# Kernel tuning notes

Hardware: AMD Instinct MI355X
Metric: run time of the kernel (lower is better)

The kernel has to match this reference:

```python
import jax, jax.numpy as jnp
import numpy as np

B, D_IN, D_HID, D_OUT, E = 8192, 1024, 4096, 1024, 8


def setup_inputs() -> dict:
    key = jax.random.key(0)
    ks = jax.random.split(key, 6)
    s_in = 1.0 / np.sqrt(D_IN)
    s_gh = 1.0 / np.sqrt(D_HID // 2)
    s_eh = 1.0 / np.sqrt(D_HID)
    return {
        "x": jax.random.normal(ks[0], (B, D_IN), jnp.float32),
        "gW1": jax.random.normal(ks[1], (D_IN, D_HID // 2), jnp.float32) * s_in,
        "gb1": jnp.zeros((D_HID // 2,), jnp.float32),
        "gW2": jax.random.normal(ks[2], (D_HID // 2, E), jnp.float32) * s_gh,
        "gb2": jnp.zeros((E,), jnp.float32),
        "eW1": jax.random.normal(ks[3], (E, D_IN, D_HID), jnp.float32) * s_in,
        "eb1": jnp.zeros((E, D_HID), jnp.float32),
        "eW2": jax.random.normal(ks[4], (E, D_HID, D_OUT), jnp.float32) * s_eh,
        "eb2": jnp.zeros((E, D_OUT), jnp.float32),
    }


def reference(x, gW1, gb1, gW2, gb2, eW1, eb1, eW2, eb2):
    # Gating network: Linear -> ReLU -> (Dropout: eval identity) -> Linear -> Softmax(dim=1)
    gh = jax.nn.relu(x @ gW1 + gb1)                      # [B, H/2]
    gates = jax.nn.softmax(gh @ gW2 + gb2, axis=1)       # [B, E]

    # All experts run on the full batch (dense MoE): batched GEMMs over expert axis.
    h = jax.nn.relu(jnp.einsum('bi,eih->beh', x, eW1) + eb1)   # [B, E, H]
    eo = jnp.einsum('beh,eho->beo', h, eW2) + eb2              # [B, E, O]

    # Gated weighted sum over experts.
    combined = jnp.einsum('beo,be->bo', eo, gates)             # [B, O]
    return (combined, gates, gates)
```

## Files before the change

kernel.cpp:

```cpp
#include <hip/hip_runtime.h>
#include <hip/hip_bf16.h>
#include <stdint.h>

#define BB 8192
#define DIN 1024
#define DHID 4096
#define DOUT 1024
#define NEXP 8
#define GH_N 2048

typedef __attribute__((ext_vector_type(8))) __bf16 bf16x8;
typedef __attribute__((ext_vector_type(4))) float f32x4;

__device__ inline unsigned short f2bf(float f) {
  unsigned u = __builtin_bit_cast(unsigned, f);
  u = (u + 0x7FFFu + ((u >> 16) & 1u)) >> 16;
  return (unsigned short)u;
}
__device__ inline float b2f(unsigned short s) {
  return __builtin_bit_cast(float, (unsigned)s << 16);
}

__global__ void cvt_f32_bf16(const float* __restrict__ in,
                             unsigned short* __restrict__ out, int n4) {
  int i = blockIdx.x * blockDim.x + threadIdx.x;
  if (i >= n4) return;
  float4 v = ((const float4*)in)[i];
  ushort4 o;
  o.x = f2bf(v.x); o.y = f2bf(v.y); o.z = f2bf(v.z); o.w = f2bf(v.w);
  ((ushort4*)out)[i] = o;
}

__device__ inline void tr_tile64(const float* __restrict__ in,
                                 unsigned short* __restrict__ out, int R, int C,
                                 int bx, int by) {
  __shared__ float tile[64][65];
  const int c0 = bx * 64, r0 = by * 64;
  const int tx = threadIdx.x & 63, ty = threadIdx.x >> 6;
#pragma unroll
  for (int i = 0; i < 16; ++i) {
    int r = i * 4 + ty;
    tile[r][tx] = in[(size_t)(r0 + r) * C + c0 + tx];
  }
  __syncthreads();
#pragma unroll
  for (int i = 0; i < 16; ++i) {
    int r = i * 4 + ty;
    out[(size_t)(c0 + r) * R + r0 + tx] = f2bf(tile[tx][r]);
  }
}

__global__ void transpose_cvt64(const float* __restrict__ in,
                                unsigned short* __restrict__ out, int R, int C) {
  tr_tile64(in, out, R, C, blockIdx.x, blockIdx.y);
}

__global__ void transpose_cvt2(const float* __restrict__ w1,
                               unsigned short* __restrict__ w1T,
                               const float* __restrict__ w2,
                               unsigned short* __restrict__ w2T) {
  int b = blockIdx.x;
  if (b < 1024) {
    tr_tile64(w1, w1T, DIN, DHID, b & 63, b >> 6);
  } else {
    b -= 1024;
    tr_tile64(w2, w2T, DHID, DOUT, b & 15, b >> 4);
  }
}

__device__ inline void gload16(const void* g, void* l) {
  __builtin_amdgcn_global_load_lds(
      (const __attribute__((address_space(1))) void*)g,
      (__attribute__((address_space(3))) void*)l, 16, 0, 0);
}

template <int N>
__device__ inline void waitv() {
  if constexpr (N == 0) asm volatile("s_waitcnt vmcnt(0)" ::: "memory");
  else if constexpr (N == 2) asm volatile("s_waitcnt vmcnt(2)" ::: "memory");
  else if constexpr (N == 4) asm volatile("s_waitcnt vmcnt(4)" ::: "memory");
  else if constexpr (N == 6) asm volatile("s_waitcnt vmcnt(6)" ::: "memory");
  else asm volatile("s_waitcnt vmcnt(0)" ::: "memory");
}
__device__ inline void waitlgkm0() {
  asm volatile("s_waitcnt lgkmcnt(0)" ::: "memory");
  __builtin_amdgcn_sched_barrier(0);
}
__device__ inline bf16x8 ldr(const char* p) { return *(const bf16x8*)p; }

struct GArgs {
  const unsigned short* A;
  const unsigned short* Bt;
  int lda, ldb, N, K;
  const float* bias;
  unsigned short* outb;
  int nb;
};

__global__ __launch_bounds__(512, 2)
void gemmU(GArgs g) {
  __shared__ char lds[131072];
  char* Als = lds;
  char* Bls = lds + 65536;
  constexpr int ABYTES = 32768, BBYTES = 32768;
  const int t = threadIdx.x;
  const int lane = t & 63;
  const int wid = t >> 6;
  const int wm = wid >> 2;
  const int wn = wid & 3;
  const int l15 = lane & 15, lg = lane >> 4;

  const int nb = g.nb;
  const int local = blockIdx.x;
  const int swz = (local & 7) * (nb >> 3) + (local >> 3);
  const int nbn = g.N >> 8;
  const int bn = swz % nbn, bm = swz / nbn;
  const int m0 = bm * 256, n0 = bn * 256;

  const int prow = t >> 3;
  const int cOff = ((t & 7) ^ (prow & 7)) * 8;
  const unsigned short* aP[4];
  const unsigned short* bP[4];
#pragma unroll
  for (int u = 0; u < 4; ++u) {
    int p = u * 64 + prow;
    int ga = ((p >> 6) & 1) * 128 + ((p >> 7) & 1) * 64 + (p & 63);
    aP[u] = g.A + (size_t)(m0 + ga) * g.lda + cOff;
    int gb = ((p >> 5) & 3) * 64 + ((p >> 7) & 1) * 32 + (p & 31);
    bP[u] = g.Bt + (size_t)(n0 + gb) * g.ldb + cOff;
  }
  const int ldst = t * 16;

  const int slot0 = ((lg) ^ (l15 & 7)) * 16;
  const int slot1 = ((4 + lg) ^ (l15 & 7)) * 16;
  const int aRB0 = (wm * 64 + l15) * 128;
  const int aRB1 = (128 + wm * 64 + l15) * 128;
  const int bCB0 = (wn * 32 + l15) * 128;
  const int bCB1 = (128 + wn * 32 + l15) * 128;

  f32x4 acc[8][4];
  const f32x4 zero = {0.f, 0.f, 0.f, 0.f};
#pragma unroll
  for (int i = 0; i < 8; ++i)
#pragma unroll
    for (int j = 0; j < 4; ++j) acc[i][j] = zero;

  bf16x8 ar[4][2], bc0[2][2], bc1[2][2];
  const int NT = g.K >> 6;

  gload16(bP[0], Bls + 0 * 8192 + ldst);
  gload16(bP[1], Bls + 1 * 8192 + ldst);
  gload16(aP[0], Als + 0 * 8192 + ldst);
  gload16(aP[1], Als + 1 * 8192 + ldst);
  gload16(bP[2], Bls + 2 * 8192 + ldst);
  gload16(bP[3], Bls + 3 * 8192 + ldst);
  gload16(aP[2], Als + 2 * 8192 + ldst);
  gload16(aP[3], Als + 3 * 8192 + ldst);
  waitv<4>();
  __builtin_amdgcn_s_barrier();

  for (int T = 0; T < NT; ++T) {
    const int buf = T & 1;
    const char* Ab = Als + buf * ABYTES;
    const char* Bb = Bls + buf * BBYTES;
    char* An = Als + (buf ^ 1) * ABYTES;
    char* Bn = Bls + (buf ^ 1) * BBYTES;
    const bool stg = (T + 1 < NT);
    const int kn = (T + 1) << 6;

#pragma unroll
    for (int f = 0; f < 4; ++f) {
      ar[f][0] = ldr(Ab + aRB0 + f * 2048 + slot0);
      ar[f][1] = ldr(Ab + aRB0 + f * 2048 + slot1);
    }
#pragma unroll
    for (int c = 0; c < 2; ++c) {
      bc0[c][0] = ldr(Bb + bCB0 + c * 2048 + slot0);
      bc0[c][1] = ldr(Bb + bCB0 + c * 2048 + slot1);
    }
    if (stg) {
      gload16(bP[0] + kn, Bn + 0 * 8192 + ldst);
      gload16(bP[1] + kn, Bn + 1 * 8192 + ldst);
    }
    __builtin_amdgcn_s_barrier();
    waitlgkm0();
    __builtin_amdgcn_s_setprio(1);
#pragma unroll
    for (int ksl = 0; ksl < 2; ++ksl)
#pragma unroll
      for (int f = 0; f < 4; ++f)
#pragma unroll
        for (int c = 0; c < 2; ++c)
          acc[f][c] = __builtin_amdgcn_mfma_f32_16x16x32_bf16(
              ar[f][ksl], bc0[c][ksl], acc[f][c], 0, 0, 0);
    __builtin_amdgcn_s_setprio(0);
    if (stg) waitv<4>(); else waitv<2>();
    __builtin_amdgcn_s_barrier();

#pragma unroll
    for (int c = 0; c < 2; ++c) {
      bc1[c][0] = ldr(Bb + bCB1 + c * 2048 + slot0);
      bc1[c][1] = ldr(Bb + bCB1 + c * 2048 + slot1);
    }
    if (stg) {
      gload16(aP[0] + kn, An + 0 * 8192 + ldst);
      gload16(aP[1] + kn, An + 1 * 8192 + ldst);
    }
    __builtin_amdgcn_s_barrier();
    waitlgkm0();
    __builtin_amdgcn_s_setprio(1);
#pragma unroll
    for (int ksl = 0; ksl < 2; ++ksl)
#pragma unroll
      for (int f = 0; f < 4; ++f)
#pragma unroll
        for (int c = 0; c < 2; ++c)
          acc[f][2 + c] = __builtin_amdgcn_mfma_f32_16x16x32_bf16(
              ar[f][ksl], bc1[c][ksl], acc[f][2 + c], 0, 0, 0);
    __builtin_amdgcn_s_setprio(0);
    if (stg) waitv<4>(); else waitv<0>();
    __builtin_amdgcn_s_barrier();

#pragma unroll
    for (int f = 0; f < 4; ++f) {
      ar[f][0] = ldr(Ab + aRB1 + f * 2048 + slot0);
      ar[f][1] = ldr(Ab + aRB1 + f * 2048 + slot1);
    }
    if (stg) {
      gload16(bP[2] + kn, Bn + 2 * 8192 + ldst);
      gload16(bP[3] + kn, Bn + 3 * 8192 + ldst);
    }
    __builtin_amdgcn_s_barrier();
    waitlgkm0();
    __builtin_amdgcn_s_setprio(1);
#pragma unroll
    for (int ksl = 0; ksl < 2; ++ksl)
#pragma unroll
      for (int f = 0; f < 4; ++f)
#pragma unroll
        for (int c = 0; c < 2; ++c)
          acc[4 + f][2 + c] = __builtin_amdgcn_mfma_f32_16x16x32_bf16(
              ar[f][ksl], bc1[c][ksl], acc[4 + f][2 + c], 0, 0, 0);
    __builtin_amdgcn_s_setprio(0);
    __builtin_amdgcn_s_barrier();

    if (stg) {
      gload16(aP[2] + kn, An + 2 * 8192 + ldst);
      gload16(aP[3] + kn, An + 3 * 8192 + ldst);
    }
    __builtin_amdgcn_s_barrier();
    __builtin_amdgcn_s_setprio(1);
#pragma unroll
    for (int ksl = 0; ksl < 2; ++ksl)
#pragma unroll
      for (int f = 0; f < 4; ++f)
#pragma unroll
        for (int c = 0; c < 2; ++c)
          acc[4 + f][c] = __builtin_amdgcn_mfma_f32_16x16x32_bf16(
              ar[f][ksl], bc0[c][ksl], acc[4 + f][c], 0, 0, 0);
    __builtin_amdgcn_s_setprio(0);
    if (stg) waitv<4>();
    __builtin_amdgcn_s_barrier();
  }

  const int rb = m0 + wm * 128 + (lg << 2);
  const int cb = n0 + wn * 64 + l15;
  const int N = g.N;
#pragma unroll
  for (int fg = 0; fg < 8; ++fg) {
#pragma unroll
    for (int j = 0; j < 4; ++j) {
      int col = cb + j * 16;
      float bv = g.bias[col];
#pragma unroll
      for (int r = 0; r < 4; ++r) {
        int row = rb + fg * 16 + r;
        float v = acc[fg][j][r] + bv;
        g.outb[(size_t)row * N + col] = f2bf(fmaxf(v, 0.f));
      }
    }
  }
}

__global__ __launch_bounds__(512)
void gemmF(const unsigned short* __restrict__ A,
           const unsigned short* __restrict__ Bt,
           const float* __restrict__ bias,
           float* __restrict__ outC,
           const float* __restrict__ gates, int eidx, int accum) {
  constexpr int SLOT = 49152;
  __shared__ char lds[3 * SLOT];
  const int t = threadIdx.x;
  const int lane = t & 63;
  const int wid = t >> 6;
  const int wm = wid >> 2;
  const int wn = wid & 3;
  const int l15 = lane & 15, lg = lane >> 4;

  const int local = blockIdx.x;
  const int swz = (local & 7) * 32 + (local >> 3);
  const int bn = swz & 3, bm = swz >> 2;
  const int m0 = bm * 128, n0 = bn * 256;

  const int prow = t >> 3;
  const int cOff = ((t & 7) ^ (prow & 7)) * 8;
  const unsigned short* aP[2];
  const unsigned short* bP[4];
#pragma unroll
  for (int u = 0; u < 2; ++u)
    aP[u] = A + (size_t)(m0 + u * 64 + prow) * DHID + cOff;
#pragma unroll
  for (int u = 0; u < 4; ++u) {
    int p = u * 64 + prow;
    int gb = ((p >> 5) & 3) * 64 + ((p >> 7) & 1) * 32 + (p & 31);
    bP[u] = Bt + (size_t)(n0 + gb) * DHID + cOff;
  }
  const int ldst = t * 16;

  const int slot0 = ((lg) ^ (l15 & 7)) * 16;
  const int slot1 = ((4 + lg) ^ (l15 & 7)) * 16;
  const int aRB = (wm * 64 + l15) * 128;
  const int bCB0 = 16384 + (wn * 32 + l15) * 128;
  const int bCB1 = 16384 + (128 + wn * 32 + l15) * 128;

  f32x4 acc[4][4];
  const f32x4 zero = {0.f, 0.f, 0.f, 0.f};
#pragma unroll
  for (int i = 0; i < 4; ++i)
#pragma unroll
    for (int j = 0; j < 4; ++j) acc[i][j] = zero;

  bf16x8 af[2][2], bc[4][2];
  const int NT = DHID >> 6;

#pragma unroll
  for (int T0 = 0; T0 < 2; ++T0) {
    char* S = lds + T0 * SLOT;
    const int k0 = T0 << 6;
    gload16(aP[0] + k0, S + 0 * 8192 + ldst);
    gload16(aP[1] + k0, S + 1 * 8192 + ldst);
    gload16(bP[0] + k0, S + 16384 + 0 * 8192 + ldst);
    gload16(bP[1] + k0, S + 16384 + 1 * 8192 + ldst);
    gload16(bP[2] + k0, S + 16384 + 2 * 8192 + ldst);
    gload16(bP[3] + k0, S + 16384 + 3 * 8192 + ldst);
  }
  waitv<6>();
  __builtin_amdgcn_s_barrier();

  for (int T = 0; T < NT; ++T) {
    const char* Sb = lds + (T % 3) * SLOT;
    char* Sn = lds + ((T + 2) % 3) * SLOT;
    const bool stg = (T + 2 < NT);
    const int kn = (T + 2) << 6;

#pragma unroll
    for (int f = 0; f < 2; ++f) {
      af[f][0] = ldr(Sb + aRB + f * 2048 + slot0);
      af[f][1] = ldr(Sb + aRB + f * 2048 + slot1);
    }
#pragma unroll
    for (int c = 0; c < 2; ++c) {
      bc[c][0] = ldr(Sb + bCB0 + c * 2048 + slot0);
      bc[c][1] = ldr(Sb + bCB0 + c * 2048 + slot1);
      bc[2 + c][0] = ldr(Sb + bCB1 + c * 2048 + slot0);
      bc[2 + c][1] = ldr(Sb + bCB1 + c * 2048 + slot1);
    }
    if (stg) {
      gload16(aP[0] + kn, Sn + 0 * 8192 + ldst);
      gload16(aP[1] + kn, Sn + 1 * 8192 + ldst);
      gload16(bP[0] + kn, Sn + 16384 + 0 * 8192 + ldst);
    }
    __builtin_amdgcn_s_barrier();
    waitlgkm0();
    __builtin_amdgcn_s_setprio(1);
#pragma unroll
    for (int ksl = 0; ksl < 2; ++ksl)
#pragma unroll
      for (int f = 0; f < 2; ++f)
#pragma unroll
        for (int c = 0; c < 4; ++c)
          acc[f][c] = __builtin_amdgcn_mfma_f32_16x16x32_bf16(
              af[f][ksl], bc[c][ksl], acc[f][c], 0, 0, 0);
    __builtin_amdgcn_s_setprio(0);
    __builtin_amdgcn_s_barrier();

#pragma unroll
    for (int f = 0; f < 2; ++f) {
      af[f][0] = ldr(Sb + aRB + (2 + f) * 2048 + slot0);
      af[f][1] = ldr(Sb + aRB + (2 + f) * 2048 + slot1);
    }
    if (stg) {
      gload16(bP[1] + kn, Sn + 16384 + 1 * 8192 + ldst);
      gload16(bP[2] + kn, Sn + 16384 + 2 * 8192 + ldst);
      gload16(bP[3] + kn, Sn + 16384 + 3 * 8192 + ldst);
    }
    __builtin_amdgcn_s_barrier();
    waitlgkm0();
    __builtin_amdgcn_s_setprio(1);
#pragma unroll
    for (int ksl = 0; ksl < 2; ++ksl)
#pragma unroll
      for (int f = 0; f < 2; ++f)
#pragma unroll
        for (int c = 0; c < 4; ++c)
          acc[2 + f][c] = __builtin_amdgcn_mfma_f32_16x16x32_bf16(
              af[f][ksl], bc[c][ksl], acc[2 + f][c], 0, 0, 0);
    __builtin_amdgcn_s_setprio(0);
    if (stg) waitv<6>();
    else if (T + 1 < NT) waitv<0>();
    __builtin_amdgcn_s_barrier();
  }

  const int rb = m0 + wm * 64 + (lg << 2);
  const int cb = n0 + wn * 64 + l15;
#pragma unroll
  for (int fg = 0; fg < 4; ++fg) {
    float gv[4];
#pragma unroll
    for (int r = 0; r < 4; ++r)
      gv[r] = gates[(size_t)(rb + fg * 16 + r) * NEXP + eidx];
#pragma unroll
    for (int j = 0; j < 4; ++j) {
      int col = cb + j * 16;
      float bv = bias[col];
#pragma unroll
      for (int r = 0; r < 4; ++r) {
        size_t o = (size_t)(rb + fg * 16 + r) * DOUT + col;
        float v = (acc[fg][j][r] + bv) * gv[r];
        outC[o] = accum ? outC[o] + v : v;
      }
    }
  }
}

__global__ __launch_bounds__(512)
void gating_head2(const unsigned short* __restrict__ gh,
                  const float* __restrict__ gW2,
                  const float* __restrict__ gb2,
                  float* __restrict__ gws,
                  float* __restrict__ g1,
                  float* __restrict__ g2) {
  __shared__ float wT[8][2048];
  const int t = threadIdx.x;
  for (int idx = t; idx < 16384; idx += 512) {
    wT[idx & 7][idx >> 3] = gW2[idx];
  }
  __syncthreads();
  const int wid = t >> 6, lane = t & 63;
  const int row = blockIdx.x * 8 + wid;
  const unsigned short* ghr = gh + (size_t)row * 2048;
  float s[8] = {0.f, 0.f, 0.f, 0.f, 0.f, 0.f, 0.f, 0.f};
#pragma unroll
  for (int j = 0; j < 8; ++j) {
    int k4 = lane + 64 * j;
    ushort4 hv = ((const ushort4*)ghr)[k4];
    float h0 = b2f(hv.x), h1 = b2f(hv.y), h2 = b2f(hv.z), h3 = b2f(hv.w);
#pragma unroll
    for (int e = 0; e < 8; ++e) {
      float4 w = ((const float4*)&wT[e][0])[k4];
      s[e] += h0 * w.x + h1 * w.y + h2 * w.z + h3 * w.w;
    }
  }
#pragma unroll
  for (int e = 0; e < 8; ++e)
#pragma unroll
    for (int off = 1; off < 64; off <<= 1) s[e] += __shfl_xor(s[e], off, 64);
  if (lane == 0) {
    float l[8], m = -1e30f;
#pragma unroll
    for (int e = 0; e < 8; ++e) {
      l[e] = s[e] + gb2[e];
      m = fmaxf(m, l[e]);
    }
    float sum = 0.f;
#pragma unroll
    for (int e = 0; e < 8; ++e) {
      l[e] = expf(l[e] - m);
      sum += l[e];
    }
    float inv = 1.f / sum;
#pragma unroll
    for (int e = 0; e < 8; ++e) {
      float gv = l[e] * inv;
      gws[(size_t)row * 8 + e] = gv;
      g1[(size_t)row * 8 + e] = gv;
      g2[(size_t)row * 8 + e] = gv;
    }
  }
}

extern "C" void kernel_launch(void* const* d_in, const int* in_sizes, int n_in,
                              void* d_out, int out_size, void* d_ws,
                              size_t ws_size, hipStream_t stream) {
  (void)in_sizes; (void)n_in; (void)out_size; (void)ws_size;
  const float* x   = (const float*)d_in[0];
  const float* gW1 = (const float*)d_in[1];
  const float* gb1 = (const float*)d_in[2];
  const float* gW2 = (const float*)d_in[3];
  const float* gb2 = (const float*)d_in[4];
  const float* eW1 = (const float*)d_in[5];
  const float* eb1 = (const float*)d_in[6];
  const float* eW2 = (const float*)d_in[7];
  const float* eb2 = (const float*)d_in[8];

  float* outC  = (float*)d_out;
  float* outG1 = outC + (size_t)BB * DOUT;
  float* outG2 = outG1 + (size_t)BB * NEXP;

  char* ws = (char*)d_ws;
  unsigned short* xb   = (unsigned short*)(ws);
  float*          gat  = (float*)(ws + 16777216);
  unsigned short* w1T  = (unsigned short*)(ws + 17039360);
  unsigned short* w2T  = (unsigned short*)(ws + 25427968);
  unsigned short* hbuf = (unsigned short*)(ws + 33816576);
  unsigned short* gh   = hbuf;
  unsigned short* gW1T = w1T;

  cvt_f32_bf16<<<(BB * DIN / 4) / 256, 256, 0, stream>>>(x, xb, BB * DIN / 4);
  transpose_cvt64<<<dim3(GH_N / 64, DIN / 64), 256, 0, stream>>>(gW1, gW1T, DIN, GH_N);
  {
    GArgs a{xb, gW1T, DIN, DIN, GH_N, DIN, gb1, gh, 256};
    gemmU<<<256, 512, 0, stream>>>(a);
  }
  gating_head2<<<BB / 8, 512, 0, stream>>>(gh, gW2, gb2, gat, outG1, outG2);

  for (int e = 0; e < NEXP; ++e) {
    transpose_cvt2<<<2048, 256, 0, stream>>>(
        eW1 + (size_t)e * DIN * DHID, w1T, eW2 + (size_t)e * DHID * DOUT, w2T);
    {
      GArgs a{xb, w1T, DIN, DIN, DHID, DIN, eb1 + (size_t)e * DHID, hbuf, 512};
      gemmU<<<512, 512, 0, stream>>>(a);
    }
    gemmF<<<256, 512, 0, stream>>>(hbuf, w2T, eb2 + (size_t)e * DOUT, outC,
                                   gat, e, e > 0 ? 1 : 0);
  }
}
```

Measured before the change: 1.343 ms.

## Overlap next expert's weight transpose with current second GEMM via double buffering

The per-expert weight transpose/convert kernel is removed from the critical path. Expert 0's weights, together with the gating W1, are transposed in one merged prologue kernel. Each later expert's weights are transposed by extra blocks launched alongside the current expert's second GEMM, writing into ping-pong buffers. This hides transpose time behind GEMM compute, at the cost of more workspace, sharing CUs with the GEMM, and giving the transpose blocks a large static LDS allocation that limits their occupancy.

```diff
diff --git a/kernel.cpp b/kernel.cpp
--- a/kernel.cpp
+++ b/kernel.cpp
@@ -31,40 +31,39 @@
   ((ushort4*)out)[i] = o;
 }
 
-__device__ inline void tr_tile64(const float* __restrict__ in,
-                                 unsigned short* __restrict__ out, int R, int C,
-                                 int bx, int by) {
+__device__ inline void tr64(float (*tile)[65], const float* __restrict__ in,
+                            unsigned short* __restrict__ out, int R, int C,
+                            int bx, int by, int t) {
+  const int c0 = bx * 64, r0 = by * 64;
+  const int tx = t & 63, ty = t >> 6;
+#pragma unroll
+  for (int i = 0; i < 8; ++i) {
+    int r = i * 8 + ty;
+    tile[r][tx] = in[(size_t)(r0 + r) * C + c0 + tx];
+  }
+  __syncthreads();
+#pragma unroll
+  for (int i = 0; i < 8; ++i) {
+    int r = i * 8 + ty;
+    out[(size_t)(c0 + r) * R + r0 + tx] = f2bf(tile[tx][r]);
+  }
+  __syncthreads();
+}
+
+__global__ __launch_bounds__(512)
+void trans_pre(const float* __restrict__ gW1, unsigned short* __restrict__ gW1T,
+               const float* __restrict__ w1, unsigned short* __restrict__ w1T,
+               const float* __restrict__ w2, unsigned short* __restrict__ w2T) {
   __shared__ float tile[64][65];
-  const int c0 = bx * 64, r0 = by * 64;
-  const int tx = threadIdx.x & 63, ty = threadIdx.x >> 6;
-#pragma unroll
-  for (int i = 0; i < 16; ++i) {
-    int r = i * 4 + ty;
-    tile[r][tx] = in[(size_t)(r0 + r) * C + c0 + tx];
-  }
-  __syncthreads();
-#pragma unroll
-  for (int i = 0; i < 16; ++i) {
-    int r = i * 4 + ty;
-    out[(size_t)(c0 + r) * R + r0 + tx] = f2bf(tile[tx][r]);
-  }
-}
-
-__global__ void transpose_cvt64(const float* __restrict__ in,
-                                unsigned short* __restrict__ out, int R, int C) {
-  tr_tile64(in, out, R, C, blockIdx.x, blockIdx.y);
-}
-
-__global__ void transpose_cvt2(const float* __restrict__ w1,
-                               unsigned short* __restrict__ w1T,
-                               const float* __restrict__ w2,
-                               unsigned short* __restrict__ w2T) {
   int b = blockIdx.x;
-  if (b < 1024) {
-    tr_tile64(w1, w1T, DIN, DHID, b & 63, b >> 6);
+  if (b < 512) {
+    tr64(tile, gW1, gW1T, DIN, GH_N, b & 31, b >> 5, threadIdx.x);
+  } else if (b < 1536) {
+    b -= 512;
+    tr64(tile, w1, w1T, DIN, DHID, b & 63, b >> 6, threadIdx.x);
   } else {
-    b -= 1024;
-    tr_tile64(w2, w2T, DHID, DOUT, b & 15, b >> 4);
+    b -= 1536;
+    tr64(tile, w2, w2T, DHID, DOUT, b & 15, b >> 4, threadIdx.x);
   }
 }
 
@@ -282,14 +281,14 @@
   }
 }
 
-__global__ __launch_bounds__(512)
-void gemmF(const unsigned short* __restrict__ A,
-           const unsigned short* __restrict__ Bt,
-           const float* __restrict__ bias,
-           float* __restrict__ outC,
-           const float* __restrict__ gates, int eidx, int accum) {
+__device__ __forceinline__
+void gemmF_core(char* lds,
+                const unsigned short* __restrict__ A,
+                const unsigned short* __restrict__ Bt,
+                const float* __restrict__ bias,
+                float* __restrict__ outC,
+                const float* __restrict__ gates, int eidx, int accum) {
   constexpr int SLOT = 49152;
-  __shared__ char lds[3 * SLOT];
   const int t = threadIdx.x;
   const int lane = t & 63;
   const int wid = t >> 6;
@@ -428,6 +427,33 @@
         size_t o = (size_t)(rb + fg * 16 + r) * DOUT + col;
         float v = (acc[fg][j][r] + bv) * gv[r];
         outC[o] = accum ? outC[o] + v : v;
+      }
+    }
+  }
+}
+
+__global__ __launch_bounds__(512)
+void g2t(const unsigned short* __restrict__ A,
+         const unsigned short* __restrict__ Bt,
+         const float* __restrict__ bias,
+         float* __restrict__ outC,
+         const float* __restrict__ gates, int eidx, int accum,
+         const float* __restrict__ nw1, unsigned short* __restrict__ nw1T,
+         const float* __restrict__ nw2, unsigned short* __restrict__ nw2T) {
+  __shared__ char lds[147456];
+  if ((int)blockIdx.x < 256) {
+    gemmF_core(lds, A, Bt, bias, outC, gates, eidx, accum);
+  } else {
+    float(*tile)[65] = (float(*)[65])lds;
+    const int tb = (int)blockIdx.x - 256;
+#pragma unroll
+    for (int i = 0; i < 8; ++i) {
+      int ti = tb * 8 + i;
+      if (ti < 1024) {
+        tr64(tile, nw1, nw1T, DIN, DHID, ti & 63, ti >> 6, threadIdx.x);
+      } else {
+        ti -= 1024;
+        tr64(tile, nw2, nw2T, DHID, DOUT, ti & 15, ti >> 4, threadIdx.x);
       }
     }
   }
@@ -510,14 +536,16 @@
   char* ws = (char*)d_ws;
   unsigned short* xb   = (unsigned short*)(ws);
   float*          gat  = (float*)(ws + 16777216);
-  unsigned short* w1T  = (unsigned short*)(ws + 17039360);
-  unsigned short* w2T  = (unsigned short*)(ws + 25427968);
-  unsigned short* hbuf = (unsigned short*)(ws + 33816576);
+  unsigned short* w1A  = (unsigned short*)(ws + 17039360);
+  unsigned short* w1B  = (unsigned short*)(ws + 25427968);
+  unsigned short* w2A  = (unsigned short*)(ws + 33816576);
+  unsigned short* w2B  = (unsigned short*)(ws + 42205184);
+  unsigned short* hbuf = (unsigned short*)(ws + 50593792);
   unsigned short* gh   = hbuf;
-  unsigned short* gW1T = w1T;
+  unsigned short* gW1T = (unsigned short*)(ws + 50593792 + 33554432);
 
   cvt_f32_bf16<<<(BB * DIN / 4) / 256, 256, 0, stream>>>(x, xb, BB * DIN / 4);
-  transpose_cvt64<<<dim3(GH_N / 64, DIN / 64), 256, 0, stream>>>(gW1, gW1T, DIN, GH_N);
+  trans_pre<<<2560, 512, 0, stream>>>(gW1, gW1T, eW1, w1A, eW2, w2A);
   {
     GArgs a{xb, gW1T, DIN, DIN, GH_N, DIN, gb1, gh, 256};
     gemmU<<<256, 512, 0, stream>>>(a);
@@ -525,13 +553,23 @@
   gating_head2<<<BB / 8, 512, 0, stream>>>(gh, gW2, gb2, gat, outG1, outG2);
 
   for (int e = 0; e < NEXP; ++e) {
-    transpose_cvt2<<<2048, 256, 0, stream>>>(
-        eW1 + (size_t)e * DIN * DHID, w1T, eW2 + (size_t)e * DHID * DOUT, w2T);
+    unsigned short* w1cur = (e & 1) ? w1B : w1A;
+    unsigned short* w2cur = (e & 1) ? w2B : w2A;
+    unsigned short* w1nxt = (e & 1) ? w1A : w1B;
+    unsigned short* w2nxt = (e & 1) ? w2A : w2B;
     {
-      GArgs a{xb, w1T, DIN, DIN, DHID, DIN, eb1 + (size_t)e * DHID, hbuf, 512};
+      GArgs a{xb, w1cur, DIN, DIN, DHID, DIN, eb1 + (size_t)e * DHID, hbuf, 512};
       gemmU<<<512, 512, 0, stream>>>(a);
     }
-    gemmF<<<256, 512, 0, stream>>>(hbuf, w2T, eb2 + (size_t)e * DOUT, outC,
-                                   gat, e, e > 0 ? 1 : 0);
-  }
-}
+    if (e + 1 < NEXP) {
+      g2t<<<512, 512, 0, stream>>>(
+          hbuf, w2cur, eb2 + (size_t)e * DOUT, outC, gat, e, e > 0 ? 1 : 0,
+          eW1 + (size_t)(e + 1) * DIN * DHID, w1nxt,
+          eW2 + (size_t)(e + 1) * DHID * DOUT, w2nxt);
+    } else {
+      g2t<<<256, 512, 0, stream>>>(
+          hbuf, w2cur, eb2 + (size_t)e * DOUT, outC, gat, e, 1,
+          nullptr, nullptr, nullptr, nullptr);
+    }
+  }
+}
```

Result: no change. 1.346 ms (+0.2%).

## Pair second-layer expert GEMMs in one launch with separate partial accumulator

Applied to the files above, without the earlier changes.

When the workspace is large enough, experts are processed in pairs. Each expert's hidden activations go to their own buffer, and one launch runs both second-layer GEMMs (128 tiles each, 256 blocks total) through the shared 256x256 gemm core instead of a 256-block gemmF. The odd expert accumulates into a separate partial buffer, which is folded into the output in the next pair's first GEMM epilogue and by a final merge kernel. The change also adds a dedicated gating-transpose kernel and reworks the transpose to 512 threads. It trades more workspace memory and extra read-modify-write traffic on the output for fewer launches and a different second-layer kernel.

```diff
diff --git a/kernel.cpp b/kernel.cpp
--- a/kernel.cpp
+++ b/kernel.cpp
@@ -31,40 +31,42 @@
   ((ushort4*)out)[i] = o;
 }
 
-__device__ inline void tr_tile64(const float* __restrict__ in,
-                                 unsigned short* __restrict__ out, int R, int C,
-                                 int bx, int by) {
+__device__ inline void tr64(float (*tile)[65], const float* __restrict__ in,
+                            unsigned short* __restrict__ out, int R, int C,
+                            int bx, int by, int t) {
+  const int c0 = bx * 64, r0 = by * 64;
+  const int tx = t & 63, ty = t >> 6;
+#pragma unroll
+  for (int i = 0; i < 8; ++i) {
+    int r = i * 8 + ty;
+    tile[r][tx] = in[(size_t)(r0 + r) * C + c0 + tx];
+  }
+  __syncthreads();
+#pragma unroll
+  for (int i = 0; i < 8; ++i) {
+    int r = i * 8 + ty;
+    out[(size_t)(c0 + r) * R + r0 + tx] = f2bf(tile[tx][r]);
+  }
+  __syncthreads();
+}
+
+__global__ __launch_bounds__(512)
+void trans_g(const float* __restrict__ gW1, unsigned short* __restrict__ gW1T) {
   __shared__ float tile[64][65];
-  const int c0 = bx * 64, r0 = by * 64;
-  const int tx = threadIdx.x & 63, ty = threadIdx.x >> 6;
-#pragma unroll
-  for (int i = 0; i < 16; ++i) {
-    int r = i * 4 + ty;
-    tile[r][tx] = in[(size_t)(r0 + r) * C + c0 + tx];
-  }
-  __syncthreads();
-#pragma unroll
-  for (int i = 0; i < 16; ++i) {
-    int r = i * 4 + ty;
-    out[(size_t)(c0 + r) * R + r0 + tx] = f2bf(tile[tx][r]);
-  }
-}
-
-__global__ void transpose_cvt64(const float* __restrict__ in,
-                                unsigned short* __restrict__ out, int R, int C) {
-  tr_tile64(in, out, R, C, blockIdx.x, blockIdx.y);
-}
-
-__global__ void transpose_cvt2(const float* __restrict__ w1,
-                               unsigned short* __restrict__ w1T,
-                               const float* __restrict__ w2,
-                               unsigned short* __restrict__ w2T) {
+  int b = blockIdx.x;
+  tr64(tile, gW1, gW1T, DIN, GH_N, b & 31, b >> 5, threadIdx.x);
+}
+
+__global__ __launch_bounds__(512)
+void trans2(const float* __restrict__ w1, unsigned short* __restrict__ w1T,
+            const float* __restrict__ w2, unsigned short* __restrict__ w2T) {
+  __shared__ float tile[64][65];
   int b = blockIdx.x;
   if (b < 1024) {
-    tr_tile64(w1, w1T, DIN, DHID, b & 63, b >> 6);
+    tr64(tile, w1, w1T, DIN, DHID, b & 63, b >> 6, threadIdx.x);
   } else {
     b -= 1024;
-    tr_tile64(w2, w2T, DHID, DOUT, b & 15, b >> 4);
+    tr64(tile, w2, w2T, DHID, DOUT, b & 15, b >> 4, threadIdx.x);
   }
 }
 
@@ -88,18 +90,18 @@
 }
 __device__ inline bf16x8 ldr(const char* p) { return *(const bf16x8*)p; }
 
-struct GArgs {
+struct GA {
   const unsigned short* A;
   const unsigned short* Bt;
   int lda, ldb, N, K;
   const float* bias;
   unsigned short* outb;
-  int nb;
+  float* outf;
+  const float* gates;
+  int eidx, accum, nb, epi;
 };
 
-__global__ __launch_bounds__(512, 2)
-void gemmU(GArgs g) {
-  __shared__ char lds[131072];
+__device__ __forceinline__ void gemm_core(const GA& g, int local, char* lds) {
   char* Als = lds;
   char* Bls = lds + 65536;
   constexpr int ABYTES = 32768, BBYTES = 32768;
@@ -111,7 +113,6 @@
   const int l15 = lane & 15, lg = lane >> 4;
 
   const int nb = g.nb;
-  const int local = blockIdx.x;
   const int swz = (local & 7) * (nb >> 3) + (local >> 3);
   const int nbn = g.N >> 8;
   const int bn = swz % nbn, bm = swz / nbn;
@@ -266,20 +267,65 @@
   const int rb = m0 + wm * 128 + (lg << 2);
   const int cb = n0 + wn * 64 + l15;
   const int N = g.N;
-#pragma unroll
-  for (int fg = 0; fg < 8; ++fg) {
-#pragma unroll
-    for (int j = 0; j < 4; ++j) {
-      int col = cb + j * 16;
-      float bv = g.bias[col];
-#pragma unroll
-      for (int r = 0; r < 4; ++r) {
-        int row = rb + fg * 16 + r;
-        float v = acc[fg][j][r] + bv;
-        g.outb[(size_t)row * N + col] = f2bf(fmaxf(v, 0.f));
+  if (g.epi == 0) {
+#pragma unroll
+    for (int fg = 0; fg < 8; ++fg) {
+#pragma unroll
+      for (int j = 0; j < 4; ++j) {
+        int col = cb + j * 16;
+        float bv = g.bias[col];
+#pragma unroll
+        for (int r = 0; r < 4; ++r) {
+          int row = rb + fg * 16 + r;
+          float v = acc[fg][j][r] + bv;
+          g.outb[(size_t)row * N + col] = f2bf(fmaxf(v, 0.f));
+        }
       }
     }
-  }
+  } else {
+#pragma unroll
+    for (int fg = 0; fg < 8; ++fg) {
+      float gv[4];
+#pragma unroll
+      for (int r = 0; r < 4; ++r)
+        gv[r] = g.gates[(size_t)(rb + fg * 16 + r) * NEXP + g.eidx];
+#pragma unroll
+      for (int j = 0; j < 4; ++j) {
+        int col = cb + j * 16;
+        float bv = g.bias[col];
+#pragma unroll
+        for (int r = 0; r < 4; ++r) {
+          size_t o = (size_t)(rb + fg * 16 + r) * N + col;
+          float v = (acc[fg][j][r] + bv) * gv[r];
+          g.outf[o] = g.accum ? g.outf[o] + v : v;
+        }
+      }
+    }
+  }
+}
+
+__global__ __launch_bounds__(512, 2)
+void k_g1(GA g, const float4* __restrict__ mrgP, float4* __restrict__ mrgO) {
+  __shared__ char lds[131072];
+  gemm_core(g, blockIdx.x, lds);
+  if (mrgP != nullptr) {
+    size_t base = ((size_t)blockIdx.x * 512 + threadIdx.x) * 8;
+#pragma unroll
+    for (int i = 0; i < 8; ++i) {
+      float4 p = mrgP[base + i];
+      float4 o = mrgO[base + i];
+      o.x += p.x; o.y += p.y; o.z += p.z; o.w += p.w;
+      mrgO[base + i] = o;
+    }
+  }
+}
+
+__global__ __launch_bounds__(512, 2)
+void k_g2pair(GA a0, GA a1) {
+  __shared__ char lds[131072];
+  const int set = blockIdx.x & 1;
+  const GA& sel = set ? a1 : a0;
+  gemm_core(sel, (int)blockIdx.x >> 1, lds);
 }
 
 __global__ __launch_bounds__(512)
@@ -433,6 +479,14 @@
   }
 }
 
+__global__ void merge_final(const float4* __restrict__ p,
+                            float4* __restrict__ o) {
+  size_t i = (size_t)blockIdx.x * 256 + threadIdx.x;
+  float4 a = p[i], b = o[i];
+  b.x += a.x; b.y += a.y; b.z += a.z; b.w += a.w;
+  o[i] = b;
+}
+
 __global__ __launch_bounds__(512)
 void gating_head2(const unsigned short* __restrict__ gh,
                   const float* __restrict__ gW2,
@@ -492,7 +546,7 @@
 extern "C" void kernel_launch(void* const* d_in, const int* in_sizes, int n_in,
                               void* d_out, int out_size, void* d_ws,
                               size_t ws_size, hipStream_t stream) {
-  (void)in_sizes; (void)n_in; (void)out_size; (void)ws_size;
+  (void)in_sizes; (void)n_in; (void)out_size;
   const float* x   = (const float*)d_in[0];
   const float* gW1 = (const float*)d_in[1];
   const float* gb1 = (const float*)d_in[2];
@@ -508,30 +562,81 @@
   float* outG2 = outG1 + (size_t)BB * NEXP;
 
   char* ws = (char*)d_ws;
-  unsigned short* xb   = (unsigned short*)(ws);
-  float*          gat  = (float*)(ws + 16777216);
-  unsigned short* w1T  = (unsigned short*)(ws + 17039360);
-  unsigned short* w2T  = (unsigned short*)(ws + 25427968);
-  unsigned short* hbuf = (unsigned short*)(ws + 33816576);
-  unsigned short* gh   = hbuf;
-  unsigned short* gW1T = w1T;
-
-  cvt_f32_bf16<<<(BB * DIN / 4) / 256, 256, 0, stream>>>(x, xb, BB * DIN / 4);
-  transpose_cvt64<<<dim3(GH_N / 64, DIN / 64), 256, 0, stream>>>(gW1, gW1T, DIN, GH_N);
-  {
-    GArgs a{xb, gW1T, DIN, DIN, GH_N, DIN, gb1, gh, 256};
-    gemmU<<<256, 512, 0, stream>>>(a);
-  }
-  gating_head2<<<BB / 8, 512, 0, stream>>>(gh, gW2, gb2, gat, outG1, outG2);
-
-  for (int e = 0; e < NEXP; ++e) {
-    transpose_cvt2<<<2048, 256, 0, stream>>>(
-        eW1 + (size_t)e * DIN * DHID, w1T, eW2 + (size_t)e * DHID * DOUT, w2T);
+  const bool pairpath = ws_size >= (size_t)209977344;
+
+  if (pairpath) {
+    unsigned short* xb   = (unsigned short*)(ws);
+    float*          gat  = (float*)(ws + 16777216);
+    unsigned short* w1s  = (unsigned short*)(ws + 17039360);
+    unsigned short* w2A  = (unsigned short*)(ws + 25427968);
+    unsigned short* w2B  = (unsigned short*)(ws + 33816576);
+    unsigned short* hA   = (unsigned short*)(ws + 42205184);
+    unsigned short* hB   = (unsigned short*)(ws + 109314048);
+    float*          pout = (float*)(ws + 176422912);
+    unsigned short* gh   = hA;
+    unsigned short* gW1T = hB;
+
+    cvt_f32_bf16<<<(BB * DIN / 4) / 256, 256, 0, stream>>>(x, xb, BB * DIN / 4);
+    trans_g<<<512, 512, 0, stream>>>(gW1, gW1T);
     {
-      GArgs a{xb, w1T, DIN, DIN, DHID, DIN, eb1 + (size_t)e * DHID, hbuf, 512};
-      gemmU<<<512, 512, 0, stream>>>(a);
-    }
-    gemmF<<<256, 512, 0, stream>>>(hbuf, w2T, eb2 + (size_t)e * DOUT, outC,
-                                   gat, e, e > 0 ? 1 : 0);
-  }
-}
+      GA a{xb, gW1T, DIN, DIN, GH_N, DIN, gb1, gh, nullptr, nullptr, 0, 0, 256, 0};
+      k_g1<<<256, 512, 0, stream>>>(a, nullptr, nullptr);
+    }
+    gating_head2<<<BB / 8, 512, 0, stream>>>(gh, gW2, gb2, gat, outG1, outG2);
+
+    for (int p = 0; p < 4; ++p) {
+      const int e0 = 2 * p, e1 = 2 * p + 1;
+      trans2<<<2048, 512, 0, stream>>>(
+          eW1 + (size_t)e0 * DIN * DHID, w1s, eW2 + (size_t)e0 * DHID * DOUT, w2A);
+      {
+        GA a{xb, w1s, DIN, DIN, DHID, DIN, eb1 + (size_t)e0 * DHID,
+             hA, nullptr, nullptr, 0, 0, 512, 0};
+        k_g1<<<512, 512, 0, stream>>>(
+            a, p > 0 ? (const float4*)pout : nullptr, (float4*)outC);
+      }
+      trans2<<<2048, 512, 0, stream>>>(
+          eW1 + (size_t)e1 * DIN * DHID, w1s, eW2 + (size_t)e1 * DHID * DOUT, w2B);
+      {
+        GA a{xb, w1s, DIN, DIN, DHID, DIN, eb1 + (size_t)e1 * DHID,
+             hB, nullptr, nullptr, 0, 0, 512, 0};
+        k_g1<<<512, 512, 0, stream>>>(a, nullptr, nullptr);
+      }
+      {
+        GA a0{hA, w2A, DHID, DHID, DOUT, DHID, eb2 + (size_t)e0 * DOUT,
+              nullptr, outC, gat, e0, p > 0 ? 1 : 0, 128, 2};
+        GA a1{hB, w2B, DHID, DHID, DOUT, DHID, eb2 + (size_t)e1 * DOUT,
+              nullptr, pout, gat, e1, 0, 128, 2};
+        k_g2pair<<<256, 512, 0, stream>>>(a0, a1);
+      }
+    }
+    merge_final<<<BB, 256, 0, stream>>>((const float4*)pout, (float4*)outC);
+  } else {
+    unsigned short* xb   = (unsigned short*)(ws);
+    float*          gat  = (float*)(ws + 16777216);
+    unsigned short* w1T  = (unsigned short*)(ws + 17039360);
+    unsigned short* w2T  = (unsigned short*)(ws + 25427968);
+    unsigned short* hbuf = (unsigned short*)(ws + 33816576);
+    unsigned short* gh   = hbuf;
+    unsigned short* gW1T = w1T;
+
+    cvt_f32_bf16<<<(BB * DIN / 4) / 256, 256, 0, stream>>>(x, xb, BB * DIN / 4);
+    trans_g<<<512, 512, 0, stream>>>(gW1, gW1T);
+    {
+      GA a{xb, gW1T, DIN, DIN, GH_N, DIN, gb1, gh, nullptr, nullptr, 0, 0, 256, 0};
+      k_g1<<<256, 512, 0, stream>>>(a, nullptr, nullptr);
+    }
+    gating_head2<<<BB / 8, 512, 0, stream>>>(gh, gW2, gb2, gat, outG1, outG2);
+
+    for (int e = 0; e < NEXP; ++e) {
+      trans2<<<2048, 512, 0, stream>>>(
+          eW1 + (size_t)e * DIN * DHID, w1T, eW2 + (size_t)e * DHID * DOUT, w2T);
+      {
+        GA a{xb, w1T, DIN, DIN, DHID, DIN, eb1 + (size_t)e * DHID,
+             hbuf, nullptr, nullptr, 0, 0, 512, 0};
+        k_g1<<<512, 512, 0, stream>>>(a, nullptr, nullptr);
+      }
+      gemmF<<<256, 512, 0, stream>>>(hbuf, w2T, eb2 + (size_t)e * DOUT, outC,
+                                     gat, e, e > 0 ? 1 : 0);
+    }
+  }
+}
```

New measurement: 1.416 ms. +5.4%, slower.
